# Optimization experiments

Hardware: AMD Instinct MI355X
Metric: run time of the kernel (lower is better)

The kernel has to match this reference:

```python
import jax, jax.numpy as jnp
import numpy as np
from jax.ops import segment_sum

N_NODES = 50000
N_EDGES = 50000
N_GRAPHS = 1024


def _inv_deg(idx, num_segments):
    deg = segment_sum(jnp.ones(idx.shape[0], jnp.float32), idx, num_segments=num_segments)
    return jnp.where(deg > 0, 1.0 / deg, 0.0)


def hypergraph_conv(x, W, b, node_idx, edge_idx):
    # PyG HypergraphConv (use_attention=False, heads=1, hyperedge_weight=1):
    # out = D^{-1} H B^{-1} H^T (X W) + b
    D = _inv_deg(node_idx, N_NODES)   # inverse node degree [N]
    B = _inv_deg(edge_idx, N_EDGES)   # inverse hyperedge degree [E]
    xl = x @ W                         # [N, out]
    # node -> hyperedge aggregation
    edge_feat = B[:, None] * segment_sum(xl[node_idx], edge_idx, num_segments=N_EDGES)
    # hyperedge -> node aggregation
    out = D[:, None] * segment_sum(edge_feat[edge_idx], node_idx, num_segments=N_NODES)
    return out + b


def global_mean_pool(x, batch):
    s = segment_sum(x, batch, num_segments=N_GRAPHS)
    cnt = segment_sum(jnp.ones(x.shape[0], jnp.float32), batch, num_segments=N_GRAPHS)
    return s / jnp.maximum(cnt, 1.0)[:, None]


def setup_inputs() -> dict:
    key = jax.random.key(0)
    ks = jax.random.split(key, 16)
    F, H = 128, 256
    def lin(k, fi, fo):
        s = 1.0 / np.sqrt(fi)
        k1, k2 = jax.random.split(k)
        return (jax.random.uniform(k1, (fi, fo), jnp.float32, -s, s),
                jax.random.uniform(k2, (fo,), jnp.float32, -s, s))
    W1, b1 = lin(ks[0], F, H)
    W2, b2 = lin(ks[1], H, 2 * H)
    W3, b3 = lin(ks[2], 2 * H, H)
    Wl1, bl1 = lin(ks[3], H, H // 2)
    Wl2, bl2 = lin(ks[4], H // 2, 1)
    x = jax.random.normal(ks[5], (N_NODES, F), jnp.float32)
    hyperedge_index = jax.random.randint(ks[6], (2, 400000), 0, N_EDGES, jnp.int64)
    batch = jnp.sort(jax.random.randint(ks[7], (N_NODES,), 0, N_GRAPHS, jnp.int64))
    return {"x": x, "hyperedge_index": hyperedge_index, "batch": batch,
            "W1": W1, "b1": b1, "W2": W2, "b2": b2, "W3": W3, "b3": b3,
            "Wl1": Wl1, "bl1": bl1, "Wl2": Wl2, "bl2": bl2}


def reference(x, hyperedge_index, batch, W1, b1, W2, b2, W3, b3, Wl1, bl1, Wl2, bl2):
    node_idx, edge_idx = hyperedge_index[0], hyperedge_index[1]
    h = jax.nn.relu(hypergraph_conv(x, W1, b1, node_idx, edge_idx))
    h = jax.nn.relu(hypergraph_conv(h, W2, b2, node_idx, edge_idx))
    h = jax.nn.relu(hypergraph_conv(h, W3, b3, node_idx, edge_idx))
    g = global_mean_pool(h, batch)              # [G, H]
    g = jax.nn.relu(g @ Wl1 + bl1)
    out = g @ Wl2 + bl2                          # [G, 1]
    return out
```

## Files before the change

kernel.cpp:

```cpp
#include <hip/hip_runtime.h>
#include <hip/hip_bf16.h>

#define N_NODES  50000
#define N_EDGES  50000
#define N_INC    400000
#define N_GRAPHS 1024
#define M_PAD    50048
#define SEG_CAP  50176

typedef __bf16 bf16x8 __attribute__((ext_vector_type(8)));
typedef float  f32x4  __attribute__((ext_vector_type(4)));

__device__ __forceinline__ unsigned short f2bf(float f) {
    __hip_bfloat16 h = __float2bfloat16(f);
    return __builtin_bit_cast(unsigned short, h);
}
__device__ __forceinline__ float bflo(unsigned int u) {
    return __builtin_bit_cast(float, u << 16);
}
__device__ __forceinline__ float bfhi(unsigned int u) {
    return __builtin_bit_cast(float, u & 0xffff0000u);
}
__device__ __forceinline__ unsigned int packbf(float a, float b) {
    return (unsigned int)f2bf(a) | ((unsigned int)f2bf(b) << 16);
}
__device__ __forceinline__ void load_lds16(const unsigned short* g, unsigned short* l) {
    __builtin_amdgcn_global_load_lds((const __attribute__((address_space(1))) void*)g,
                                     (__attribute__((address_space(3))) void*)l, 16, 0, 0);
}

#define NB_INC  1563
__global__ __launch_bounds__(256) void normhist_kernel(const int* __restrict__ hei,
                                                       int* __restrict__ nidx, int* __restrict__ eidx,
                                                       unsigned short* __restrict__ rn,
                                                       unsigned short* __restrict__ re,
                                                       int* __restrict__ ndeg_p, int* __restrict__ edeg_p) {
    __shared__ int s32;
    int t = threadIdx.x;
    if (t == 0) s32 = 0;
    __syncthreads();
    int probe = hei[4 * t + 1] | hei[4 * t + 3];
    if (probe) s32 = 1;
    __syncthreads();
    int is32 = s32;
    int i = blockIdx.x * 256 + t;
    if (i < N_INC) {
        int n, e;
        if (is32) { n = hei[i];     e = hei[N_INC + i]; }
        else      { n = hei[2 * i]; e = hei[2 * N_INC + 2 * i]; }
        nidx[i] = n; eidx[i] = e;
        rn[i] = (unsigned short)atomicAdd(&ndeg_p[n << 4], 1);
        re[i] = (unsigned short)atomicAdd(&edeg_p[e << 4], 1);
    }
}

__global__ __launch_bounds__(256) void scan_up_f(const int* __restrict__ edeg_p,
                                                 const int* __restrict__ ndeg_p,
                                                 const int* __restrict__ hei,
                                                 const int* __restrict__ braw,
                                                 int* __restrict__ eoff, int* __restrict__ noff,
                                                 int* __restrict__ goff,
                                                 int* __restrict__ partials) {
    int b = blockIdx.x, t = threadIdx.x;
    if (b >= 98) {
        __shared__ int s32;
        if (t == 0) s32 = 0;
        __syncthreads();
        int probe = hei[4 * t + 1] | hei[4 * t + 3];
        if (probe) s32 = 1;
        __syncthreads();
        int is32 = s32;
        int g = (b - 98) * 256 + t;
        int lo = 0, hi = N_NODES;
        while (lo < hi) {
            int mid = (lo + hi) >> 1;
            int v = is32 ? braw[mid] : braw[2 * mid];
            if (v < g) lo = mid + 1; else hi = mid;
        }
        goff[g] = lo;
        if (g == 1023) goff[1024] = N_NODES;
        return;
    }
    __shared__ int lds[256];
    const int* in; int* outp; int lb;
    if (b < 49) { in = edeg_p; outp = eoff; lb = b; }
    else        { in = ndeg_p; outp = noff; lb = b - 49; }
    int base = lb * 1024 + t * 4;
    int4 v;
    v.x = in[(size_t)(base + 0) << 4];
    v.y = in[(size_t)(base + 1) << 4];
    v.z = in[(size_t)(base + 2) << 4];
    v.w = in[(size_t)(base + 3) << 4];
    int s = v.x + v.y + v.z + v.w;
    lds[t] = s;
    __syncthreads();
    for (int off = 1; off < 256; off <<= 1) {
        int u = (t >= off) ? lds[t - off] : 0;
        __syncthreads();
        lds[t] += u;
        __syncthreads();
    }
    int excl = lds[t] - s;
    if (t == 255) partials[b] = lds[255];
    int4 o;
    o.x = excl;
    o.y = excl + v.x;
    o.z = o.y + v.y;
    o.w = o.z + v.z;
    *(int4*)(outp + base) = o;
}

__global__ __launch_bounds__(256) void scan_down_f(int* __restrict__ eoff,
                                                   int* __restrict__ noff,
                                                   const int* __restrict__ partials) {
    __shared__ int lds[98];
    int b = blockIdx.x, t = threadIdx.x;
    if (t < 98) lds[t] = partials[t];
    __syncthreads();
    if (t < 2) {
        int lo = t * 49, hi = lo + 49;
        int run = 0;
        for (int i = lo; i < hi; ++i) { int x = lds[i]; lds[i] = run; run += x; }
    }
    __syncthreads();
    int* outp; int lb;
    if (b < 49) { outp = eoff; lb = b; }
    else        { outp = noff; lb = b - 49; }
    int base = lb * 1024 + t * 4;
    int p = lds[b];
    int4 v = *(const int4*)(outp + base);
    v.x += p; v.y += p; v.z += p; v.w += p;
    *(int4*)(outp + base) = v;
}

#define NB_CSR  1563
#define NB_CONV 6250
#define NB_W1   128
#define NB_W2   512
#define NB_W3   512
__global__ __launch_bounds__(256) void prep_kernel(const int* __restrict__ nidx,
                                                   const int* __restrict__ eidx,
                                                   const unsigned short* __restrict__ rn,
                                                   const unsigned short* __restrict__ re,
                                                   const int* __restrict__ eoff,
                                                   const int* __restrict__ noff,
                                                   unsigned short* __restrict__ csre,
                                                   unsigned short* __restrict__ csrn,
                                                   const float* __restrict__ x,
                                                   unsigned short* __restrict__ xbf,
                                                   const float* __restrict__ W1, unsigned short* __restrict__ wt1,
                                                   const float* __restrict__ W2, unsigned short* __restrict__ wt2,
                                                   const float* __restrict__ W3, unsigned short* __restrict__ wt3) {
    int b = blockIdx.x, t = threadIdx.x;
    if (b < NB_CSR) {
        int i = b * 256 + t;
        if (i < N_INC) {
            int n = nidx[i], e = eidx[i];
            csre[eoff[e] + re[i]] = (unsigned short)n;
            csrn[noff[n] + rn[i]] = (unsigned short)e;
        }
    } else if (b < NB_CSR + NB_CONV) {
        int i = (b - NB_CSR) * 256 + t;
        float4 v = *(const float4*)(x + 4 * (size_t)i);
        ushort4 o;
        o.x = f2bf(v.x); o.y = f2bf(v.y); o.z = f2bf(v.z); o.w = f2bf(v.w);
        *(ushort4*)(xbf + 4 * (size_t)i) = o;
    } else if (b < NB_CSR + NB_CONV + NB_W1) {
        int i = (b - NB_CSR - NB_CONV) * 256 + t;
        int k = i >> 8, n = i & 255;
        wt1[n * 128 + k] = f2bf(W1[i]);
    } else if (b < NB_CSR + NB_CONV + NB_W1 + NB_W2) {
        int i = (b - NB_CSR - NB_CONV - NB_W1) * 256 + t;
        int k = i >> 9, n = i & 511;
        wt2[n * 256 + k] = f2bf(W2[i]);
    } else {
        int i = (b - NB_CSR - NB_CONV - NB_W1 - NB_W2) * 256 + t;
        int k = i >> 8, n = i & 255;
        wt3[n * 512 + k] = f2bf(W3[i]);
    }
}

template <bool EPI>
__global__ __launch_bounds__(256) void gemm128_kernel(const unsigned short* __restrict__ A,
                                                      const unsigned short* __restrict__ Bt,
                                                      const float* __restrict__ bias,
                                                      unsigned short* __restrict__ C,
                                                      int M, int K, int N) {
    __shared__ unsigned short smem[2 * 128 * 64];
    unsigned short* As = smem;
    unsigned short* Bs = smem + 128 * 64;
    int tid  = threadIdx.x;
    int wave = tid >> 6, lane = tid & 63;

    int nx  = N >> 7;
    int nwg = gridDim.x;
    int bid = blockIdx.x;
    int q = nwg >> 3, r = nwg & 7;
    int xcd = bid & 7, loc = bid >> 3;
    int wg = (xcd < r) ? (xcd * (q + 1) + loc) : (r * (q + 1) + (xcd - r) * q + loc);
    int n0 = (wg % nx) * 128, m0 = (wg / nx) * 128;

    int quad = lane >> 4, fr = lane & 15;
    int wr = wave >> 1, wc = wave & 1;
    int lrow8 = lane >> 3;
    int lcol  = ((lane & 7) ^ lrow8) * 8;

    const unsigned short* gsrc;
    unsigned short* ldst;
    if (wave < 2) { gsrc = A  + (size_t)(m0 + wave * 64) * K;       ldst = As + wave * 64 * 64; }
    else          { gsrc = Bt + (size_t)(n0 + (wave - 2) * 64) * K; ldst = Bs + (wave - 2) * 64 * 64; }

    f32x4 acc[4][4];
#pragma unroll
    for (int s = 0; s < 4; ++s)
#pragma unroll
        for (int c = 0; c < 4; ++c) acc[s][c] = (f32x4){0.f, 0.f, 0.f, 0.f};

    int swz = fr & 7;
    for (int k0 = 0; k0 < K; k0 += 64) {
#pragma unroll
        for (int l = 0; l < 8; ++l) {
            const unsigned short* g = gsrc + (size_t)(l * 8 + lrow8) * K + k0 + lcol;
            load_lds16(g, ldst + l * 8 * 64);
        }
        __syncthreads();
#pragma unroll
        for (int kk = 0; kk < 2; ++kk) {
            int slot = (kk * 4 + quad) ^ swz;
            bf16x8 af[4], bfr[4];
#pragma unroll
            for (int s = 0; s < 4; ++s)
                af[s] = *(const bf16x8*)&As[(wr * 64 + s * 16 + fr) * 64 + slot * 8];
#pragma unroll
            for (int c = 0; c < 4; ++c)
                bfr[c] = *(const bf16x8*)&Bs[(wc * 64 + c * 16 + fr) * 64 + slot * 8];
#pragma unroll
            for (int s = 0; s < 4; ++s)
#pragma unroll
                for (int c = 0; c < 4; ++c)
                    acc[s][c] = __builtin_amdgcn_mfma_f32_16x16x32_bf16(af[s], bfr[c], acc[s][c], 0, 0, 0);
        }
        __syncthreads();
    }

    float bv[4];
#pragma unroll
    for (int c = 0; c < 4; ++c) bv[c] = EPI ? bias[n0 + wc * 64 + c * 16 + fr] : 0.f;
    unsigned short (*Cs)[136] = reinterpret_cast<unsigned short (*)[136]>(smem);
#pragma unroll
    for (int sp = 0; sp < 2; ++sp) {
#pragma unroll
        for (int sl = 0; sl < 2; ++sl) {
#pragma unroll
            for (int c = 0; c < 4; ++c)
#pragma unroll
                for (int r = 0; r < 4; ++r) {
                    float v = acc[sp * 2 + sl][c][r];
                    if (EPI) v = fmaxf(v + bv[c], 0.f);
                    Cs[sl * 32 + wr * 16 + quad * 4 + r][wc * 64 + c * 16 + fr] = f2bf(v);
                }
        }
        __syncthreads();
#pragma unroll
        for (int i = 0; i < 4; ++i) {
            int rl  = i * 16 + (tid >> 4);
            int col = (tid & 15) * 8;
            int gm  = m0 + ((rl & 31) >> 4) * 64 + (sp * 2 + (rl >> 5)) * 16 + (rl & 15);
            if (gm < M) {
                uint4 v = *(const uint4*)&Cs[rl][col];
                *(uint4*)&C[(size_t)gm * N + n0 + col] = v;
            }
        }
        __syncthreads();
    }
}

template <int C, bool BIAS>
__global__ __launch_bounds__(256) void seg_sliced_kernel(const unsigned short* __restrict__ in,
                                                         const int* __restrict__ offs,
                                                         const int* __restrict__ degs_p,
                                                         const unsigned short* __restrict__ csr_src,
                                                         const float* __restrict__ bias,
                                                         unsigned short* __restrict__ outp,
                                                         int nseg) {
    constexpr int NS = C / 32;
    int bid = blockIdx.x;
    int slice, segblock;
    if (NS == 8) { slice = bid & 7; segblock = bid >> 3; }
    else         { int x = bid & 7; slice = x & 3; segblock = ((bid >> 3) << 1) | (x >> 2); }

    int wave = threadIdx.x >> 6, lane = threadIdx.x & 63;
    int grp = lane >> 3, lg = lane & 7;
    int segbase = (segblock * 4 + wave) * 8;
    if (segbase >= nseg) return;
    int seg = segbase + grp;
    bool segvalid = seg < nseg;
    int deg   = segvalid ? degs_p[(size_t)seg << 4] : 0;
    int start = segvalid ? offs[seg] : 0;
    float dinv = (deg > 0) ? 1.0f / (float)deg : 0.0f;
    int maxdeg = deg;
#pragma unroll
    for (int m = 8; m < 64; m <<= 1) maxdeg = max(maxdeg, __shfl_xor(maxdeg, m, 64));
    const unsigned short* cs = csr_src + start;
    float acc[4] = {0.f, 0.f, 0.f, 0.f};
    size_t fbase = (size_t)slice * 32 + lg * 4;

    int dc = (deg > 0) ? deg - 1 : 0;
    int gbase = grp << 3;
    for (int j = 0; j < maxdeg; j += 8) {
        if (j < deg) {
            int my = (int)cs[min(j + lg, dc)];
            int row[8];
#pragma unroll
            for (int u = 0; u < 8; ++u) row[u] = __shfl(my, gbase + u, 64);
            uint2 v[8];
#pragma unroll
            for (int u = 0; u < 8; ++u)
                v[u] = *(const uint2*)(in + (size_t)row[u] * C + fbase);
            __asm__ __volatile__("" ::: "memory");
            if (j + 8 <= deg) {
#pragma unroll
                for (int u = 0; u < 8; ++u) {
                    acc[0] += bflo(v[u].x); acc[1] += bfhi(v[u].x);
                    acc[2] += bflo(v[u].y); acc[3] += bfhi(v[u].y);
                }
            } else {
#pragma unroll
                for (int u = 0; u < 8; ++u) {
                    unsigned int msk = (j + u < deg) ? 0xffffffffu : 0u;
                    unsigned int x0 = v[u].x & msk, x1 = v[u].y & msk;
                    acc[0] += bflo(x0); acc[1] += bfhi(x0);
                    acc[2] += bflo(x1); acc[3] += bfhi(x1);
                }
            }
        }
    }

    if (!segvalid) return;
    float a0 = acc[0] * dinv, a1 = acc[1] * dinv;
    float a2 = acc[2] * dinv, a3 = acc[3] * dinv;
    if constexpr (BIAS) {
        a0 = fmaxf(a0 + bias[fbase + 0], 0.f);
        a1 = fmaxf(a1 + bias[fbase + 1], 0.f);
        a2 = fmaxf(a2 + bias[fbase + 2], 0.f);
        a3 = fmaxf(a3 + bias[fbase + 3], 0.f);
    }
    unsigned long long ov = (unsigned long long)packbf(a0, a1)
                          | ((unsigned long long)packbf(a2, a3) << 32);
    __builtin_nontemporal_store(ov, (unsigned long long*)(outp + (size_t)seg * C + fbase));
}

__global__ __launch_bounds__(256) void pool_head_kernel(const unsigned short* __restrict__ h,
                                                        const int* __restrict__ goff,
                                                        const float* __restrict__ Wl1,
                                                        const float* __restrict__ bl1,
                                                        const float* __restrict__ Wl2,
                                                        const float* __restrict__ bl2,
                                                        float* __restrict__ out) {
    __shared__ float xs[256];
    __shared__ float red[128];
    int g = blockIdx.x, t = threadIdx.x;
    int s = goff[g], cnt = goff[g + 1] - s;
    float a0 = 0.f, a1 = 0.f, a2 = 0.f, a3 = 0.f;
    int i = 0;
    for (; i + 4 <= cnt; i += 4) {
        unsigned int u0 = h[(size_t)(s + i + 0) * 256 + t];
        unsigned int u1 = h[(size_t)(s + i + 1) * 256 + t];
        unsigned int u2 = h[(size_t)(s + i + 2) * 256 + t];
        unsigned int u3 = h[(size_t)(s + i + 3) * 256 + t];
        a0 += __builtin_bit_cast(float, u0 << 16);
        a1 += __builtin_bit_cast(float, u1 << 16);
        a2 += __builtin_bit_cast(float, u2 << 16);
        a3 += __builtin_bit_cast(float, u3 << 16);
    }
    for (; i < cnt; ++i) {
        unsigned int u = h[(size_t)(s + i) * 256 + t];
        a0 += __builtin_bit_cast(float, u << 16);
    }
    float acc = (a0 + a1) + (a2 + a3);
    xs[t] = acc / (float)(cnt > 0 ? cnt : 1);
    __syncthreads();
    if (t < 128) {
        float s2 = 0.f;
        for (int f = 0; f < 256; ++f) s2 += xs[f] * Wl1[f * 128 + t];
        s2 = fmaxf(s2 + bl1[t], 0.f);
        red[t] = s2 * Wl2[t];
    }
    __syncthreads();
    for (int off = 64; off > 0; off >>= 1) {
        if (t < off) red[t] += red[t + off];
        __syncthreads();
    }
    if (t == 0) out[g] = red[0] + bl2[0];
}

extern "C" void kernel_launch(void* const* d_in, const int* in_sizes, int n_in,
                              void* d_out, int out_size, void* d_ws, size_t ws_size,
                              hipStream_t stream) {
    const float* x     = (const float*)d_in[0];
    const int* hei     = (const int*)d_in[1];
    const int* braw    = (const int*)d_in[2];
    const float* W1    = (const float*)d_in[3];
    const float* b1    = (const float*)d_in[4];
    const float* W2    = (const float*)d_in[5];
    const float* b2    = (const float*)d_in[6];
    const float* W3    = (const float*)d_in[7];
    const float* b3    = (const float*)d_in[8];
    const float* Wl1   = (const float*)d_in[9];
    const float* bl1   = (const float*)d_in[10];
    const float* Wl2   = (const float*)d_in[11];
    const float* bl2   = (const float*)d_in[12];
    float* out         = (float*)d_out;

    char* w = (char*)d_ws;
    size_t off = 0;
    auto alloc = [&](size_t bytes) { size_t p = off; off += (bytes + 255) & ~(size_t)255; return p; };
    size_t o_edegp = alloc((size_t)SEG_CAP * 16 * 4);
    size_t o_ndegp = alloc((size_t)SEG_CAP * 16 * 4);
    size_t zero_end = off;
    size_t o_eoff = alloc((size_t)SEG_CAP * 4);
    size_t o_noff = alloc((size_t)SEG_CAP * 4);
    size_t o_goff = alloc((size_t)1025 * 4);
    size_t o_part = alloc(128 * 4);
    size_t o_nidx = alloc((size_t)N_INC * 4);
    size_t o_eidx = alloc((size_t)N_INC * 4);
    size_t o_rn   = alloc((size_t)N_INC * 2);
    size_t o_re   = alloc((size_t)N_INC * 2);
    size_t o_csre = alloc((size_t)N_INC * 2 + 64);
    size_t o_csrn = alloc((size_t)N_INC * 2 + 64);
    size_t o_wt1  = alloc((size_t)128 * 256 * 2);
    size_t o_wt2  = alloc((size_t)256 * 512 * 2);
    size_t o_wt3  = alloc((size_t)512 * 256 * 2);
    size_t o_xbf  = alloc((size_t)M_PAD * 128 * 2);
    size_t o_Y    = alloc((size_t)M_PAD * 256 * 2);
    size_t o_H1   = alloc((size_t)M_PAD * 256 * 2);
    size_t o_H2   = alloc((size_t)M_PAD * 512 * 2);
    size_t o_bufE = alloc((size_t)N_EDGES * 256 * 2);

    int* edeg_p = (int*)(w + o_edegp);
    int* ndeg_p = (int*)(w + o_ndegp);
    int* eoff = (int*)(w + o_eoff);
    int* noff = (int*)(w + o_noff);
    int* goff = (int*)(w + o_goff);
    int* part = (int*)(w + o_part);
    int* nidx = (int*)(w + o_nidx);
    int* eidx = (int*)(w + o_eidx);
    unsigned short* rn   = (unsigned short*)(w + o_rn);
    unsigned short* re   = (unsigned short*)(w + o_re);
    unsigned short* csre = (unsigned short*)(w + o_csre);
    unsigned short* csrn = (unsigned short*)(w + o_csrn);
    unsigned short* wt1  = (unsigned short*)(w + o_wt1);
    unsigned short* wt2  = (unsigned short*)(w + o_wt2);
    unsigned short* wt3  = (unsigned short*)(w + o_wt3);
    unsigned short* xbf  = (unsigned short*)(w + o_xbf);
    unsigned short* Y    = (unsigned short*)(w + o_Y);
    unsigned short* H1   = (unsigned short*)(w + o_H1);
    unsigned short* H2   = (unsigned short*)(w + o_H2);
    unsigned short* bufE = (unsigned short*)(w + o_bufE);

    hipMemsetAsync(w, 0, zero_end, stream);
    normhist_kernel<<<NB_INC, 256, 0, stream>>>(hei, nidx, eidx, rn, re, ndeg_p, edeg_p);
    scan_up_f<<<102, 256, 0, stream>>>(edeg_p, ndeg_p, hei, braw, eoff, noff, goff, part);
    scan_down_f<<<98, 256, 0, stream>>>(eoff, noff, part);
    prep_kernel<<<NB_CSR + NB_CONV + NB_W1 + NB_W2 + NB_W3, 256, 0, stream>>>(
        nidx, eidx, rn, re, eoff, noff, csre, csrn, x, xbf, W1, wt1, W2, wt2, W3, wt3);

    int sb = (N_NODES + 31) / 32;
    int grid256 = sb * 8;
    int grid128 = sb * 4;

    seg_sliced_kernel<128, false><<<grid128, 256, 0, stream>>>(xbf, eoff, edeg_p, csre, nullptr, bufE, N_EDGES);
    seg_sliced_kernel<128, false><<<grid128, 256, 0, stream>>>(bufE, noff, ndeg_p, csrn, nullptr, Y, N_NODES);
    {
        dim3 grid((256 / 128) * (M_PAD / 128));
        gemm128_kernel<true><<<grid, 256, 0, stream>>>(Y, wt1, b1, H1, N_NODES, 128, 256);
    }
    seg_sliced_kernel<256, false><<<grid256, 256, 0, stream>>>(H1, eoff, edeg_p, csre, nullptr, bufE, N_EDGES);
    seg_sliced_kernel<256, false><<<grid256, 256, 0, stream>>>(bufE, noff, ndeg_p, csrn, nullptr, Y, N_NODES);
    {
        dim3 grid((512 / 128) * (M_PAD / 128));
        gemm128_kernel<true><<<grid, 256, 0, stream>>>(Y, wt2, b2, H2, N_NODES, 256, 512);
    }
    {
        dim3 grid((256 / 128) * (M_PAD / 128));
        gemm128_kernel<false><<<grid, 256, 0, stream>>>(H2, wt3, nullptr, Y, N_NODES, 512, 256);
    }
    seg_sliced_kernel<256, false><<<grid256, 256, 0, stream>>>(Y, eoff, edeg_p, csre, nullptr, bufE, N_EDGES);
    seg_sliced_kernel<256, true><<<grid256, 256, 0, stream>>>(bufE, noff, ndeg_p, csrn, b3, H1, N_NODES);

    pool_head_kernel<<<N_GRAPHS, 256, 0, stream>>>(H1, goff, Wl1, bl1, Wl2, bl2, out);
}
```

Baseline: 465.0 us.

## Store node/edge feature matrices in 32-column sliced layout for locality

Feature buffers are laid out as separate 32-column slices, each a contiguous [rows x 32] block, instead of row-major. All producers and consumers use the new indexing: the conversion kernel, the GEMM A loads and C stores, the segment-sum kernels and the pooling head. Each slice-parallel segment kernel then gathers from a compact region, which is meant to improve cache and TLB locality for the random row gathers. Degrees now come from CSR offset differences rather than the padded degree array, which drops one strided load per segment.

```diff
diff --git a/kernel.cpp b/kernel.cpp
--- a/kernel.cpp
+++ b/kernel.cpp
@@ -7,6 +7,7 @@
 #define N_GRAPHS 1024
 #define M_PAD    50048
 #define SEG_CAP  50176
+#define RS ((size_t)M_PAD * 32)
 
 typedef __bf16 bf16x8 __attribute__((ext_vector_type(8)));
 typedef float  f32x4  __attribute__((ext_vector_type(4)));
@@ -164,7 +165,8 @@
         float4 v = *(const float4*)(x + 4 * (size_t)i);
         ushort4 o;
         o.x = f2bf(v.x); o.y = f2bf(v.y); o.z = f2bf(v.z); o.w = f2bf(v.w);
-        *(ushort4*)(xbf + 4 * (size_t)i) = o;
+        int row = i >> 5, f = (i & 31) * 4;
+        *(ushort4*)(xbf + (size_t)(f >> 5) * RS + (size_t)row * 32 + (f & 31)) = o;
     } else if (b < NB_CSR + NB_CONV + NB_W1) {
         int i = (b - NB_CSR - NB_CONV) * 256 + t;
         int k = i >> 8, n = i & 255;
@@ -205,10 +207,10 @@
     int lrow8 = lane >> 3;
     int lcol  = ((lane & 7) ^ lrow8) * 8;
 
-    const unsigned short* gsrc;
-    unsigned short* ldst;
-    if (wave < 2) { gsrc = A  + (size_t)(m0 + wave * 64) * K;       ldst = As + wave * 64 * 64; }
-    else          { gsrc = Bt + (size_t)(n0 + (wave - 2) * 64) * K; ldst = Bs + (wave - 2) * 64 * 64; }
+    bool isA = wave < 2;
+    int rbase = isA ? (m0 + wave * 64) : (n0 + (wave - 2) * 64);
+    const unsigned short* gsB = Bt + (size_t)rbase * K;
+    unsigned short* ldst = isA ? (As + wave * 64 * 64) : (Bs + (wave - 2) * 64 * 64);
 
     f32x4 acc[4][4];
 #pragma unroll
@@ -220,7 +222,13 @@
     for (int k0 = 0; k0 < K; k0 += 64) {
 #pragma unroll
         for (int l = 0; l < 8; ++l) {
-            const unsigned short* g = gsrc + (size_t)(l * 8 + lrow8) * K + k0 + lcol;
+            const unsigned short* g;
+            if (isA) {
+                int kk = k0 + lcol;
+                g = A + (size_t)(kk >> 5) * RS + (size_t)(rbase + l * 8 + lrow8) * 32 + (kk & 31);
+            } else {
+                g = gsB + (size_t)(l * 8 + lrow8) * K + k0 + lcol;
+            }
             load_lds16(g, ldst + l * 8 * 64);
         }
         __syncthreads();
@@ -268,7 +276,8 @@
             int gm  = m0 + ((rl & 31) >> 4) * 64 + (sp * 2 + (rl >> 5)) * 16 + (rl & 15);
             if (gm < M) {
                 uint4 v = *(const uint4*)&Cs[rl][col];
-                *(uint4*)&C[(size_t)gm * N + n0 + col] = v;
+                int f = n0 + col;
+                *(uint4*)&C[(size_t)(f >> 5) * RS + (size_t)gm * 32 + (f & 31)] = v;
             }
         }
         __syncthreads();
@@ -278,7 +287,6 @@
 template <int C, bool BIAS>
 __global__ __launch_bounds__(256) void seg_sliced_kernel(const unsigned short* __restrict__ in,
                                                          const int* __restrict__ offs,
-                                                         const int* __restrict__ degs_p,
                                                          const unsigned short* __restrict__ csr_src,
                                                          const float* __restrict__ bias,
                                                          unsigned short* __restrict__ outp,
@@ -295,15 +303,15 @@
     if (segbase >= nseg) return;
     int seg = segbase + grp;
     bool segvalid = seg < nseg;
-    int deg   = segvalid ? degs_p[(size_t)seg << 4] : 0;
     int start = segvalid ? offs[seg] : 0;
+    int deg   = segvalid ? (offs[seg + 1] - start) : 0;
     float dinv = (deg > 0) ? 1.0f / (float)deg : 0.0f;
     int maxdeg = deg;
 #pragma unroll
     for (int m = 8; m < 64; m <<= 1) maxdeg = max(maxdeg, __shfl_xor(maxdeg, m, 64));
     const unsigned short* cs = csr_src + start;
+    const unsigned short* sbase = in + (size_t)slice * RS;
     float acc[4] = {0.f, 0.f, 0.f, 0.f};
-    size_t fbase = (size_t)slice * 32 + lg * 4;
 
     int dc = (deg > 0) ? deg - 1 : 0;
     int gbase = grp << 3;
@@ -316,7 +324,7 @@
             uint2 v[8];
 #pragma unroll
             for (int u = 0; u < 8; ++u)
-                v[u] = *(const uint2*)(in + (size_t)row[u] * C + fbase);
+                v[u] = *(const uint2*)(sbase + (size_t)row[u] * 32 + lg * 4);
             __asm__ __volatile__("" ::: "memory");
             if (j + 8 <= deg) {
 #pragma unroll
@@ -340,14 +348,16 @@
     float a0 = acc[0] * dinv, a1 = acc[1] * dinv;
     float a2 = acc[2] * dinv, a3 = acc[3] * dinv;
     if constexpr (BIAS) {
-        a0 = fmaxf(a0 + bias[fbase + 0], 0.f);
-        a1 = fmaxf(a1 + bias[fbase + 1], 0.f);
-        a2 = fmaxf(a2 + bias[fbase + 2], 0.f);
-        a3 = fmaxf(a3 + bias[fbase + 3], 0.f);
+        size_t fb = (size_t)slice * 32 + lg * 4;
+        a0 = fmaxf(a0 + bias[fb + 0], 0.f);
+        a1 = fmaxf(a1 + bias[fb + 1], 0.f);
+        a2 = fmaxf(a2 + bias[fb + 2], 0.f);
+        a3 = fmaxf(a3 + bias[fb + 3], 0.f);
     }
     unsigned long long ov = (unsigned long long)packbf(a0, a1)
                           | ((unsigned long long)packbf(a2, a3) << 32);
-    __builtin_nontemporal_store(ov, (unsigned long long*)(outp + (size_t)seg * C + fbase));
+    __builtin_nontemporal_store(ov,
+        (unsigned long long*)(outp + (size_t)slice * RS + (size_t)seg * 32 + lg * 4));
 }
 
 __global__ __launch_bounds__(256) void pool_head_kernel(const unsigned short* __restrict__ h,
@@ -361,20 +371,21 @@
     __shared__ float red[128];
     int g = blockIdx.x, t = threadIdx.x;
     int s = goff[g], cnt = goff[g + 1] - s;
+    const unsigned short* hb = h + (size_t)(t >> 5) * RS + (t & 31);
     float a0 = 0.f, a1 = 0.f, a2 = 0.f, a3 = 0.f;
     int i = 0;
     for (; i + 4 <= cnt; i += 4) {
-        unsigned int u0 = h[(size_t)(s + i + 0) * 256 + t];
-        unsigned int u1 = h[(size_t)(s + i + 1) * 256 + t];
-        unsigned int u2 = h[(size_t)(s + i + 2) * 256 + t];
-        unsigned int u3 = h[(size_t)(s + i + 3) * 256 + t];
+        unsigned int u0 = hb[(size_t)(s + i + 0) * 32];
+        unsigned int u1 = hb[(size_t)(s + i + 1) * 32];
+        unsigned int u2 = hb[(size_t)(s + i + 2) * 32];
+        unsigned int u3 = hb[(size_t)(s + i + 3) * 32];
         a0 += __builtin_bit_cast(float, u0 << 16);
         a1 += __builtin_bit_cast(float, u1 << 16);
         a2 += __builtin_bit_cast(float, u2 << 16);
         a3 += __builtin_bit_cast(float, u3 << 16);
     }
     for (; i < cnt; ++i) {
-        unsigned int u = h[(size_t)(s + i) * 256 + t];
+        unsigned int u = hb[(size_t)(s + i) * 32];
         a0 += __builtin_bit_cast(float, u << 16);
     }
     float acc = (a0 + a1) + (a2 + a3);
@@ -431,11 +442,11 @@
     size_t o_wt1  = alloc((size_t)128 * 256 * 2);
     size_t o_wt2  = alloc((size_t)256 * 512 * 2);
     size_t o_wt3  = alloc((size_t)512 * 256 * 2);
-    size_t o_xbf  = alloc((size_t)M_PAD * 128 * 2);
-    size_t o_Y    = alloc((size_t)M_PAD * 256 * 2);
-    size_t o_H1   = alloc((size_t)M_PAD * 256 * 2);
-    size_t o_H2   = alloc((size_t)M_PAD * 512 * 2);
-    size_t o_bufE = alloc((size_t)N_EDGES * 256 * 2);
+    size_t o_xbf  = alloc(RS * 4 * 2);
+    size_t o_Y    = alloc(RS * 8 * 2);
+    size_t o_H1   = alloc(RS * 8 * 2);
+    size_t o_H2   = alloc(RS * 16 * 2);
+    size_t o_bufE = alloc(RS * 8 * 2);
 
     int* edeg_p = (int*)(w + o_edegp);
     int* ndeg_p = (int*)(w + o_ndegp);
@@ -469,14 +480,14 @@
     int grid256 = sb * 8;
     int grid128 = sb * 4;
 
-    seg_sliced_kernel<128, false><<<grid128, 256, 0, stream>>>(xbf, eoff, edeg_p, csre, nullptr, bufE, N_EDGES);
-    seg_sliced_kernel<128, false><<<grid128, 256, 0, stream>>>(bufE, noff, ndeg_p, csrn, nullptr, Y, N_NODES);
+    seg_sliced_kernel<128, false><<<grid128, 256, 0, stream>>>(xbf, eoff, csre, nullptr, bufE, N_EDGES);
+    seg_sliced_kernel<128, false><<<grid128, 256, 0, stream>>>(bufE, noff, csrn, nullptr, Y, N_NODES);
     {
         dim3 grid((256 / 128) * (M_PAD / 128));
         gemm128_kernel<true><<<grid, 256, 0, stream>>>(Y, wt1, b1, H1, N_NODES, 128, 256);
     }
-    seg_sliced_kernel<256, false><<<grid256, 256, 0, stream>>>(H1, eoff, edeg_p, csre, nullptr, bufE, N_EDGES);
-    seg_sliced_kernel<256, false><<<grid256, 256, 0, stream>>>(bufE, noff, ndeg_p, csrn, nullptr, Y, N_NODES);
+    seg_sliced_kernel<256, false><<<grid256, 256, 0, stream>>>(H1, eoff, csre, nullptr, bufE, N_EDGES);
+    seg_sliced_kernel<256, false><<<grid256, 256, 0, stream>>>(bufE, noff, csrn, nullptr, Y, N_NODES);
     {
         dim3 grid((512 / 128) * (M_PAD / 128));
         gemm128_kernel<true><<<grid, 256, 0, stream>>>(Y, wt2, b2, H2, N_NODES, 256, 512);
@@ -485,8 +496,8 @@
         dim3 grid((256 / 128) * (M_PAD / 128));
         gemm128_kernel<false><<<grid, 256, 0, stream>>>(H2, wt3, nullptr, Y, N_NODES, 512, 256);
     }
-    seg_sliced_kernel<256, false><<<grid256, 256, 0, stream>>>(Y, eoff, edeg_p, csre, nullptr, bufE, N_EDGES);
-    seg_sliced_kernel<256, true><<<grid256, 256, 0, stream>>>(bufE, noff, ndeg_p, csrn, b3, H1, N_NODES);
+    seg_sliced_kernel<256, false><<<grid256, 256, 0, stream>>>(Y, eoff, csre, nullptr, bufE, N_EDGES);
+    seg_sliced_kernel<256, true><<<grid256, 256, 0, stream>>>(bufE, noff, csrn, b3, H1, N_NODES);
 
     pool_head_kernel<<<N_GRAPHS, 256, 0, stream>>>(H1, goff, Wl1, bl1, Wl2, bl2, out);
 }
```

Measured after the change: 430.8 us. -7.4%, faster.
